# Kernel optimization log

Hardware: AMD Instinct MI355X
Metric: run time of the kernel (lower is better)

Reference implementation:

```python
import jax, jax.numpy as jnp
import numpy as np

F = 128          # feature_size
N = 512          # num_vertices (batch_size fixed to 1 by the original indexing)
C = 32 * 7 * 7 * 7   # 10976, f2 channel dim
G = 13           # f2 spatial grid (indices = (v+1)*6 in [0,12])
EPS = 1e-5


def _block(x, W1, b1, W2, b2, g, be, m, v):
    # Linear -> ELU -> Linear -> ELU -> Dropout(eval=id) -> BatchNorm1d(eval)
    h = jax.nn.elu(x @ W1 + b1)
    h = jax.nn.elu(h @ W2 + b2)
    return (h - m) * (g * jax.lax.rsqrt(v + EPS)) + be


def setup_inputs() -> dict:
    key = jax.random.key(0)
    ks = iter(jax.random.split(key, 80))

    def nrm(sh, s):
        return jax.random.normal(next(ks), sh, jnp.float32) * s

    def lin(i, o):
        return nrm((i, o), 1.0 / np.sqrt(i)), nrm((o,), 0.01)

    def bn():
        g = 1.0 + nrm((F,), 0.05)
        be = nrm((F,), 0.05)
        m = nrm((F,), 0.1)
        v = jax.random.uniform(next(ks), (F,), jnp.float32) + 0.5
        return g, be, m, v

    d = {}
    d['vertices'] = jax.random.uniform(next(ks), (1, N, 3), jnp.float32) * 2.0 - 1.0
    d['f2'] = nrm((1, G, G, G, C), 0.1)
    ii = jnp.arange(N, dtype=jnp.int32)
    d['v1s_idx'] = jnp.repeat(ii, N)   # edge k=(i,j): i = k//N
    d['v2s_idx'] = jnp.tile(ii, N)     #               j = k%N
    d['adj'] = (jax.random.uniform(next(ks), (N, N)) < 0.05).astype(jnp.float32)

    for p, (i, o) in [('mv', (3, F)), ('mf', (C, F)), ('s1', (2 * F, F)),
                      ('s2', (F, F)), ('s3', (2 * F, F))]:
        W1, b1 = lin(i, o)
        W2, b2 = lin(F, F)
        g, be, m, v = bn()
        d.update({p + '_W1': W1, p + '_b1': b1, p + '_W2': W2, p + '_b2': b2,
                  p + '_g': g, p + '_be': be, p + '_m': m, p + '_v': v})
    W3, b3 = lin(F, 2)
    d['s3_W3'], d['s3_b3'] = W3, b3
    return d


def _forward(vertices, f2, adj,
             mv_W1, mv_b1, mv_W2, mv_b2, mv_g, mv_be, mv_m, mv_v,
             mf_W1, mf_b1, mf_W2, mf_b2, mf_g, mf_be, mf_m, mf_v,
             s1_W1, s1_b1, s1_W2, s1_b2, s1_g, s1_be, s1_m, s1_v,
             s2_W1, s2_b1, s2_W2, s2_b2, s2_g, s2_be, s2_m, s2_v,
             s3_W1, s3_b1, s3_W2, s3_b2, s3_g, s3_be, s3_m, s3_v, s3_W3, s3_b3,
             v1s_idx, v2s_idx):
    b, n, _ = vertices.shape
    flat = vertices.reshape(-1, 3)                        # (B*N, 3)
    idx = ((flat + 1.0) * 6.0).astype(jnp.int32)          # grid indices in [0,12]
    f2e = f2[0, idx[:, 0], idx[:, 1], idx[:, 2], :]       # gather: (B*N, C)
    vf = _block(flat, mv_W1, mv_b1, mv_W2, mv_b2, mv_g, mv_be, mv_m, mv_v)
    ff = _block(f2e, mf_W1, mf_b1, mf_W2, mf_b2, mf_g, mf_be, mf_m, mf_v)
    vert = jnp.concatenate([vf, ff], -1).reshape(b, n, 2 * F)  # (B, N, 2F)

    # stage1: NodeToEdge (endpoint combine) -> MLP block over all N^2 edges
    e1 = vert[:, v1s_idx] + vert[:, v2s_idx]              # (B, N*N, 2F)
    s1 = _block(e1, s1_W1, s1_b1, s1_W2, s1_b2, s1_g, s1_be, s1_m, s1_v)  # (B, E, F)

    # stage2: EdgeToNode (adjacency-masked sum) -> MLP -> NodeToEdge
    nodes = jnp.einsum('bijf,ij->bif', s1.reshape(b, n, n, F), adj)  # (B, N, F)
    n2 = _block(nodes, s2_W1, s2_b1, s2_W2, s2_b2, s2_g, s2_be, s2_m, s2_v)
    s2 = n2[:, v1s_idx] + n2[:, v2s_idx]                  # (B, E, F)

    cat = jnp.concatenate([s1, s2], -1).reshape(b * n * n, 2 * F)
    h = _block(cat, s3_W1, s3_b1, s3_W2, s3_b2, s3_g, s3_be, s3_m, s3_v)
    return (h @ s3_W3 + s3_b3).reshape(b, n, n, 2)


def reference(vertices, f2, v1s_idx, v2s_idx, adj,
              mv_W1, mv_b1, mv_W2, mv_b2, mv_g, mv_be, mv_m, mv_v,
              mf_W1, mf_b1, mf_W2, mf_b2, mf_g, mf_be, mf_m, mf_v,
              s1_W1, s1_b1, s1_W2, s1_b2, s1_g, s1_be, s1_m, s1_v,
              s2_W1, s2_b1, s2_W2, s2_b2, s2_g, s2_be, s2_m, s2_v,
              s3_W1, s3_b1, s3_W2, s3_b2, s3_g, s3_be, s3_m, s3_v, s3_W3, s3_b3):
    return _forward(vertices, f2, adj,
                    mv_W1, mv_b1, mv_W2, mv_b2, mv_g, mv_be, mv_m, mv_v,
                    mf_W1, mf_b1, mf_W2, mf_b2, mf_g, mf_be, mf_m, mf_v,
                    s1_W1, s1_b1, s1_W2, s1_b2, s1_g, s1_be, s1_m, s1_v,
                    s2_W1, s2_b1, s2_W2, s2_b2, s2_g, s2_be, s2_m, s2_v,
                    s3_W1, s3_b1, s3_W2, s3_b2, s3_g, s3_be, s3_m, s3_v, s3_W3, s3_b3,
                    v1s_idx, v2s_idx)
```

## Files before the change

### kernel.cpp

```cpp
#include <hip/hip_runtime.h>
#include <hip/hip_bf16.h>


#define F    128
#define NV   512
#define CCC  10976
#define EPSV 1e-5f

typedef __attribute__((ext_vector_type(8)))  short        short8;
typedef __attribute__((ext_vector_type(4)))  float        f32x4;
typedef __attribute__((ext_vector_type(4)))  float        flt4;
typedef __attribute__((ext_vector_type(4)))  unsigned int u32x4;

union Frag { u32x4 q; short8 s; unsigned int d[4]; unsigned short u[8]; };

__device__ __forceinline__ unsigned short f2bf(float x){
  union { float f; unsigned int u; } c; c.f = x;
  unsigned int r = c.u + 0x7FFFu + ((c.u >> 16) & 1u);
  return (unsigned short)(r >> 16);
}
__device__ __forceinline__ unsigned int pkbf(float a, float b){
  union { __hip_bfloat162 h; unsigned int u; } cv;
  cv.h = __float22bfloat162_rn(make_float2(a, b));
  return cv.u;
}
__device__ __forceinline__ float eluf(float x){
  return x > 0.f ? x : (__expf(x) - 1.f);
}
__device__ __forceinline__ f32x4 mfma16(short8 a, short8 b, f32x4 c){
  return __builtin_amdgcn_mfma_f32_16x16x32_bf16(a, b, c, 0, 0, 0);
}

#define WS_U      0u
#define WS_FFPRE  262144u
#define WS_NODES  524288u
#define WS_WPERM  786432u
#define WS_ADJS   1048576u
#define WS_CNT    1050624u
#define WS_PJ     1052672u
#define WS_VEC    1183744u
#define WS_W2FS1  1188864u
#define WS_W1AFS3 1221632u
#define WS_W2FS3  1254400u
#define WS_W3F    1287168u
#define WS_MFW1F  1291264u
#define WS_END    4101120u
#define WS_PART   4101120u
#define WS_PART_END 15373312u


__global__ __launch_bounds__(256) void k_setup(
    const float* s1W2, const float* s3W1, const float* s3W2, const float* s3W3,
    const float* __restrict__ mfW1,
    const float* s1g, const float* s1be, const float* s1m, const float* s1v,
    const float* s3g, const float* s3be, const float* s3m, const float* s3v,
    const float* s1b2, const float* s3b2, const float* __restrict__ adj,
    unsigned short* w2fs1, unsigned short* w1afs3, unsigned short* w2fs3,
    unsigned short* w3f, unsigned short* __restrict__ mfw1f,
    float* vec, float* zeroreg,
    unsigned short* __restrict__ pj, int* __restrict__ cntI,
    float* __restrict__ cntF)
{
  __shared__ float sm[32 * 132];
  __shared__ unsigned long long msk[8];
  int bid = blockIdx.x, tid = threadIdx.x;

  if (bid < 460){
    int t = bid * 256 + tid;
    if (t < 49152){
      int T = t >> 14, tt = t & 16383;
      int e = tt & 7, lane = (tt >> 3) & 63, grp = tt >> 9;
      int slot = (grp >> 3) * 32 + ((lane >> 4) & 3) * 8 + e;
      int col  = (grp & 7) * 16 + (lane & 15);
      float val;
      unsigned short* dst;
      if (T == 0){ dst = w2fs1; val = s1W2[slot * F + col]; }
      else {
        int kf = (slot & 7) * 16 + (slot >> 3);
        if (T == 1){
          float sc1 = s1g[kf] * rsqrtf(s1v[kf] + EPSV);
          dst = w1afs3; val = sc1 * s3W1[kf * F + col];
        } else {
          dst = w2fs3; val = s3W2[kf * F + col];
        }
      }
      dst[tt] = f2bf(val);
      return;
    }
    t -= 49152;
    if (t < 2048){
      int e = t & 7, lane = (t >> 3) & 63, ks = t >> 9;
      int slot = ks * 32 + ((lane >> 4) & 3) * 8 + e;
      int kf = (slot & 7) * 16 + (slot >> 3);
      int n = lane & 15;
      float sc3 = s3g[kf] * rsqrtf(s3v[kf] + EPSV);
      w3f[t] = f2bf(n < 2 ? sc3 * s3W3[kf * 2 + n] : 0.f);
      return;
    }
    t -= 2048;
    if (t < 1024){
      int f = t & 127, which = t >> 7;
      int s = (f & 15) * 8 + (f >> 4);
      switch (which){
        case 0: vec[512 + s] = s1b2[f]; break;
        case 1: vec[640 + s] = s3b2[f]; break;
        case 2: vec[768 + f] = s1g[f] * rsqrtf(s1v[f] + EPSV); break;
        case 3: vec[896 + f] = s1be[f] - s1m[f] * (s1g[f] * rsqrtf(s1v[f] + EPSV)); break;
        case 4: {
          float a = 0.f;
          for (int k = 0; k < F; ++k){
            float sc = s1g[k] * rsqrtf(s1v[k] + EPSV);
            a = fmaf(s1be[k] - s1m[k] * sc, s3W1[k * F + f], a);
          }
          vec[1024 + f] = a;
        } break;
        case 5: if (f < 16){
          float a = 0.f;
          if (f < 2){
            for (int k = 0; k < F; ++k){
              float sc = s3g[k] * rsqrtf(s3v[k] + EPSV);
              a = fmaf(s3be[k] - s3m[k] * sc, s3W3[k * 2 + f], a);
            }
          }
          vec[1152 + f] = a;
        } break;
        default: break;
      }
      return;
    }
    t -= 1024;
    if (t < 65536) zeroreg[t] = 0.f;
    return;
  }

  if (bid < 803){
    int ksg = bid - 460;
    const float* src = mfW1 + ksg * 32 * F;
    #pragma unroll
    for (int p = 0; p < 4; ++p){
      int g4 = tid + p * 256;
      int row = g4 >> 5, col = (g4 & 31) * 4;
      flt4 v = *(const flt4*)(src + row * F + col);
      *(flt4*)(sm + row * 132 + col) = v;
    }
    __syncthreads();
    unsigned int* dst = (unsigned int*)mfw1f + ksg * 2048;
    #pragma unroll
    for (int q2 = 0; q2 < 8; ++q2){
      int o = (tid * 8 + q2) * 2;
      int nt = o >> 9, lane = (o >> 3) & 63, e = o & 7;
      int k = (lane >> 4) * 8 + e;
      int n = nt * 16 + (lane & 15);
      dst[tid * 8 + q2] = pkbf(sm[k * 132 + n], sm[(k + 1) * 132 + n]);
    }
    return;
  }

  {
    int i = bid - 803, wv = tid >> 6, ln = tid & 63;
    bool p0 = adj[i * NV + tid] != 0.f;
    bool p1 = adj[i * NV + 256 + tid] != 0.f;
    unsigned long long m0 = __ballot(p0);
    unsigned long long m1 = __ballot(p1);
    if (ln == 0){ msk[wv] = m0; msk[4 + wv] = m1; }
    __syncthreads();
    int base0 = 0, base1 = 0, tot = 0;
    #pragma unroll
    for (int g = 0; g < 8; ++g){
      int c = __popcll(msk[g]);
      if (g < wv) base0 += c;
      if (g < 4 + wv) base1 += c;
      tot += c;
    }
    unsigned long long below = (1ull << ln) - 1ull;
    if (p0){
      int r = base0 + __popcll(m0 & below);
      if (r < 128) pj[i * 128 + r] = (unsigned short)tid;
    }
    if (p1){
      int r = base1 + __popcll(m1 & below);
      if (r < 128) pj[i * 128 + r] = (unsigned short)(256 + tid);
    }
    if (tid == 0){ cntI[i] = tot > 128 ? 128 : tot; cntF[i] = (float)tot; }
  }
}

__global__ __launch_bounds__(256) void k_ff1(
    const float* __restrict__ verts, const float* __restrict__ f2,
    const unsigned short* __restrict__ mfw1f, float* __restrict__ ffpre,
    float* __restrict__ partials, int use_parts)
{
  int tid = threadIdx.x, w = tid >> 6, l = tid & 63, g = l >> 4, mm = l & 15;
  int mb = blockIdx.x & 7, kc = blockIdx.x >> 3;
  int v = mb * 64 + w * 16 + mm;
  float x0 = verts[v * 3 + 0], x1 = verts[v * 3 + 1], x2 = verts[v * 3 + 2];
  int i0 = (int)((x0 + 1.f) * 6.f), i1 = (int)((x1 + 1.f) * 6.f), i2 = (int)((x2 + 1.f) * 6.f);
  int base = ((i0 * 13 + i1) * 13 + i2) * CCC;

  f32x4 zero = {0.f, 0.f, 0.f, 0.f};
  f32x4 acc[8];
  #pragma unroll
  for (int nt = 0; nt < 8; ++nt) acc[nt] = zero;

  const u32x4* bt = (const u32x4*)mfw1f;
  #pragma unroll
  for (int kk = 0; kk < 8; ++kk){
    int ksg = kc * 8 + kk;
    if (ksg >= 343) break;
    const float* ap = f2 + base + ksg * 32 + g * 8;
    flt4 a0 = *(const flt4*)ap;
    flt4 a1 = *(const flt4*)(ap + 4);
    Frag a;
    a.d[0] = pkbf(a0.x, a0.y); a.d[1] = pkbf(a0.z, a0.w);
    a.d[2] = pkbf(a1.x, a1.y); a.d[3] = pkbf(a1.z, a1.w);
    #pragma unroll
    for (int nt = 0; nt < 8; ++nt){
      Frag b; b.q = bt[(ksg * 8 + nt) * 64 + l];
      acc[nt] = mfma16(a.s, b.s, acc[nt]);
    }
  }
  if (use_parts){
    #pragma unroll
    for (int nt = 0; nt < 8; ++nt){
      int n = nt * 16 + mm;
      #pragma unroll
      for (int r = 0; r < 4; ++r)
        partials[(kc * NV + mb * 64 + w * 16 + g * 4 + r) * F + n] = acc[nt][r];
    }
  } else {
    #pragma unroll
    for (int nt = 0; nt < 8; ++nt){
      int n = nt * 16 + mm;
      #pragma unroll
      for (int r = 0; r < 4; ++r)
        atomicAdd(&ffpre[(mb * 64 + w * 16 + g * 4 + r) * F + n], acc[nt][r]);
    }
  }
}

__global__ __launch_bounds__(128) void k_vert(
    const float* __restrict__ verts, const float* __restrict__ ffpre,
    const float* __restrict__ partials, int use_parts,
    const float* mvW1, const float* mvb1, const float* mvW2, const float* mvb2,
    const float* mvg, const float* mvbe, const float* mvm, const float* mvv,
    const float* mfb1, const float* mfW2, const float* mfb2,
    const float* mfg, const float* mfbe, const float* mfm, const float* mfv,
    const float* s1W1, const float* s1b1, float* __restrict__ uP)
{
  __shared__ float hv[F], hf[F], vf[F], ff[F];
  int f = threadIdx.x, v = blockIdx.x;
  float x0 = verts[v * 3], x1 = verts[v * 3 + 1], x2 = verts[v * 3 + 2];
  hv[f] = eluf(mvb1[f] + x0 * mvW1[f] + x1 * mvW1[F + f] + x2 * mvW1[2 * F + f]);
  float fp;
  if (use_parts){
    fp = 0.f;
    for (int kc = 0; kc < 43; ++kc) fp += partials[(kc * NV + v) * F + f];
  } else {
    fp = ffpre[v * F + f];
  }
  hf[f] = eluf(fp + mfb1[f]);
  __syncthreads();
  float sv = mvb2[f], sf = mfb2[f];
  for (int k = 0; k < F; ++k){
    sv = fmaf(hv[k], mvW2[k * F + f], sv);
    sf = fmaf(hf[k], mfW2[k * F + f], sf);
  }
  vf[f] = (eluf(sv) - mvm[f]) * (mvg[f] * rsqrtf(mvv[f] + EPSV)) + mvbe[f];
  ff[f] = (eluf(sf) - mfm[f]) * (mfg[f] * rsqrtf(mfv[f] + EPSV)) + mfbe[f];
  __syncthreads();
  float u = 0.5f * s1b1[f];
  for (int k = 0; k < F; ++k){
    u = fmaf(vf[k], s1W1[k * F + f], u);
    u = fmaf(ff[k], s1W1[(128 + k) * F + f], u);
  }
  uP[v * F + f] = u;
}

__global__ __launch_bounds__(256) void k_pass1s(
    const float* __restrict__ uP, const unsigned short* __restrict__ w2fs1,
    const float* __restrict__ vec, const unsigned short* __restrict__ pj,
    const int* __restrict__ cntA, float* __restrict__ nodes)
{
  __shared__ u32x4 Wb[2048];
  __shared__ float ci[F], nblk[F];
  int tid = threadIdx.x, i = blockIdx.x;
  int cnt = cntA[i];
  { const u32x4* ws_ = (const u32x4*)w2fs1;
    #pragma unroll
    for (int ii = 0; ii < 8; ++ii) Wb[tid + 256 * ii] = ws_[tid + 256 * ii]; }
  if (tid < F){ ci[tid] = uP[i * F + tid]; nblk[tid] = 0.f; }
  __syncthreads();

  int w = tid >> 6, l = tid & 63, g = l >> 4, mm = l & 15;
  float b2v[8];
  *(flt4*)&b2v[0] = *(const flt4*)(vec + 512 + mm * 8);
  *(flt4*)&b2v[4] = *(const flt4*)(vec + 516 + mm * 8);

  for (int t = 0; t * 64 < cnt; ++t){
    int row = t * 64 + w * 16 + mm;
    int j = (row < cnt) ? (int)pj[i * 128 + row] : 0;
    f32x4 acc[8];
    #pragma unroll
    for (int nt = 0; nt < 8; ++nt){ float b = b2v[nt]; acc[nt] = (f32x4){b, b, b, b}; }
    #pragma unroll
    for (int ks = 0; ks < 4; ++ks){
      int kb = ks * 32 + g * 8;
      flt4 ua = *(const flt4*)(uP + j * F + kb);
      flt4 ub = *(const flt4*)(uP + j * F + kb + 4);
      flt4 c0 = *(const flt4*)&ci[kb];
      flt4 c1 = *(const flt4*)&ci[kb + 4];
      Frag a;
      a.d[0] = pkbf(eluf(ua.x + c0.x), eluf(ua.y + c0.y));
      a.d[1] = pkbf(eluf(ua.z + c0.z), eluf(ua.w + c0.w));
      a.d[2] = pkbf(eluf(ub.x + c1.x), eluf(ub.y + c1.y));
      a.d[3] = pkbf(eluf(ub.z + c1.z), eluf(ub.w + c1.w));
      #pragma unroll
      for (int nt = 0; nt < 8; ++nt){
        Frag b; b.q = Wb[(ks * 8 + nt) * 64 + l];
        acc[nt] = mfma16(a.s, b.s, acc[nt]);
      }
    }
    int rbase = t * 64 + w * 16 + g * 4;
    float mk[4];
    #pragma unroll
    for (int r = 0; r < 4; ++r) mk[r] = (rbase + r < cnt) ? 1.f : 0.f;
    #pragma unroll
    for (int nt = 0; nt < 8; ++nt){
      float s = mk[0] * eluf(acc[nt][0]);
      s = fmaf(mk[1], eluf(acc[nt][1]), s);
      s = fmaf(mk[2], eluf(acc[nt][2]), s);
      s = fmaf(mk[3], eluf(acc[nt][3]), s);
      s += __shfl_xor(s, 16, 64);
      s += __shfl_xor(s, 32, 64);
      if (l < 16) atomicAdd(&nblk[nt * 16 + mm], s);
    }
  }
  __syncthreads();
  if (tid < F) nodes[i * F + tid] = nblk[tid];
}

__global__ __launch_bounds__(128) void k_mid(
    const float* __restrict__ nodes, const float* __restrict__ cntF,
    const float* __restrict__ vec,
    const float* s2W1, const float* s2b1, const float* s2W2, const float* s2b2,
    const float* s2g, const float* s2be, const float* s2m, const float* s2v,
    const float* s3W1, const float* s3b1, float* __restrict__ wPp)
{
  __shared__ float a[F], b[F];
  int f = threadIdx.x, r = blockIdx.x;
  a[f] = vec[768 + f] * nodes[r * F + f] + vec[896 + f] * cntF[r];
  __syncthreads();
  float s = s2b1[f];
  for (int k = 0; k < F; ++k) s = fmaf(a[k], s2W1[k * F + f], s);
  b[f] = eluf(s);
  __syncthreads();
  float s2 = s2b2[f];
  for (int k = 0; k < F; ++k) s2 = fmaf(b[k], s2W2[k * F + f], s2);
  float n2 = (eluf(s2) - s2m[f]) * (s2g[f] * rsqrtf(s2v[f] + EPSV)) + s2be[f];
  __syncthreads();
  a[f] = n2;
  __syncthreads();
  float wv = 0.5f * (s3b1[f] + vec[1024 + f]);
  for (int k = 0; k < F; ++k) wv = fmaf(a[k], s3W1[(128 + k) * F + f], wv);
  wPp[r * F + ((f & 15) * 8 + (f >> 4))] = wv;
}

__global__ __launch_bounds__(256, 2) void k_pass3(
    const float* __restrict__ uP, const float* __restrict__ wPp,
    const unsigned short* __restrict__ w2fs1, const unsigned short* __restrict__ w1afs3,
    const unsigned short* __restrict__ w2fs3, const unsigned short* __restrict__ w3f,
    const float* __restrict__ vec, const float* __restrict__ s3b3,
    float* __restrict__ out)
{
  __shared__ u32x4 Wb[2048];
  __shared__ __align__(16) char Hb[32768];
  __shared__ float ci[F];
  int tid = threadIdx.x, bid = blockIdx.x;
  int band, idx;
  if (bid < 512)      { band = 0; idx = bid; }
  else if (bid < 896) { band = 1; idx = bid - 512; }
  else if (bid < 1152){ band = 2; idx = bid - 896; }
  else                { band = 3; idx = bid - 1152; }
  int tpb = 4 - band;
  int i  = band * 128 + idx / tpb;
  int j0 = (band + idx % tpb) * 128;

  int w = tid >> 6, l = tid & 63, g = l >> 4, mm = l & 15;
  char* hb = Hb + w * 8192;
  int jbase = j0 + w * 32;
  int sx = (mm & 7) << 4;

  { const u32x4* ws_ = (const u32x4*)w2fs1;
    #pragma unroll
    for (int ii = 0; ii < 8; ++ii) Wb[tid + 256 * ii] = ws_[tid + 256 * ii]; }
  if (tid < F) ci[tid] = uP[i * F + tid];
  __syncthreads();

  f32x4 acc[2][8];
  {
    float b2v[8];
    *(flt4*)&b2v[0] = *(const flt4*)(vec + 512 + mm * 8);
    *(flt4*)&b2v[4] = *(const flt4*)(vec + 516 + mm * 8);
    #pragma unroll
    for (int m = 0; m < 2; ++m)
    #pragma unroll
    for (int nt = 0; nt < 8; ++nt){ float b = b2v[nt]; acc[m][nt] = (f32x4){b, b, b, b}; }
  }
  #pragma unroll
  for (int ks = 0; ks < 4; ++ks){
    int kb = ks * 32 + g * 8;
    flt4 c0 = *(const flt4*)&ci[kb];
    flt4 c1 = *(const flt4*)&ci[kb + 4];
    Frag a0, a1;
    {
      const float* p0 = uP + (jbase + mm) * F + kb;
      flt4 ua = *(const flt4*)p0;
      flt4 ub = *(const flt4*)(p0 + 4);
      a0.d[0] = pkbf(eluf(ua.x + c0.x), eluf(ua.y + c0.y));
      a0.d[1] = pkbf(eluf(ua.z + c0.z), eluf(ua.w + c0.w));
      a0.d[2] = pkbf(eluf(ub.x + c1.x), eluf(ub.y + c1.y));
      a0.d[3] = pkbf(eluf(ub.z + c1.z), eluf(ub.w + c1.w));
      const float* p1 = uP + (jbase + 16 + mm) * F + kb;
      flt4 va = *(const flt4*)p1;
      flt4 vb = *(const flt4*)(p1 + 4);
      a1.d[0] = pkbf(eluf(va.x + c0.x), eluf(va.y + c0.y));
      a1.d[1] = pkbf(eluf(va.z + c0.z), eluf(va.w + c0.w));
      a1.d[2] = pkbf(eluf(vb.x + c1.x), eluf(vb.y + c1.y));
      a1.d[3] = pkbf(eluf(vb.z + c1.z), eluf(vb.w + c1.w));
    }
    #pragma unroll
    for (int nt = 0; nt < 8; ++nt){
      Frag b; b.q = Wb[(ks * 8 + nt) * 64 + l];
      acc[0][nt] = mfma16(a0.s, b.s, acc[0][nt]);
      acc[1][nt] = mfma16(a1.s, b.s, acc[1][nt]);
    }
  }
  #pragma unroll
  for (int m = 0; m < 2; ++m)
  #pragma unroll
  for (int r = 0; r < 4; ++r){
    int row = m * 16 + g * 4 + r;
    u32x4 wd;
    #pragma unroll
    for (int q = 0; q < 4; ++q)
      wd[q] = pkbf(eluf(acc[m][2*q][r]), eluf(acc[m][2*q+1][r]));
    *(u32x4*)(hb + row * 256 + ((mm * 16) ^ ((row & 7) << 4))) = wd;
  }
  __syncthreads();
  { const u32x4* ws_ = (const u32x4*)w1afs3;
    #pragma unroll
    for (int ii = 0; ii < 8; ++ii) Wb[tid + 256 * ii] = ws_[tid + 256 * ii]; }
  __syncthreads();

  {
    float wiv[8];
    *(flt4*)&wiv[0] = *(const flt4*)(wPp + i * F + mm * 8);
    *(flt4*)&wiv[4] = *(const flt4*)(wPp + i * F + mm * 8 + 4);
    #pragma unroll
    for (int m = 0; m < 2; ++m)
    #pragma unroll
    for (int nt = 0; nt < 8; ++nt){ float b = wiv[nt]; acc[m][nt] = (f32x4){b, b, b, b}; }
  }
  #pragma unroll
  for (int ks = 0; ks < 4; ++ks){
    Frag a0; a0.q = *(const u32x4*)(hb + mm * 256 + ((ks * 64 + g * 16) ^ sx));
    Frag a1; a1.q = *(const u32x4*)(hb + (16 + mm) * 256 + ((ks * 64 + g * 16) ^ sx));
    #pragma unroll
    for (int nt = 0; nt < 8; ++nt){
      Frag b; b.q = Wb[(ks * 8 + nt) * 64 + l];
      acc[0][nt] = mfma16(a0.s, b.s, acc[0][nt]);
      acc[1][nt] = mfma16(a1.s, b.s, acc[1][nt]);
    }
  }
  #pragma unroll
  for (int m = 0; m < 2; ++m)
  #pragma unroll
  for (int r = 0; r < 4; ++r){
    int row = m * 16 + g * 4 + r;
    int jj = jbase + row;
    float wjv[8];
    *(flt4*)&wjv[0] = *(const flt4*)(wPp + jj * F + mm * 8);
    *(flt4*)&wjv[4] = *(const flt4*)(wPp + jj * F + mm * 8 + 4);
    u32x4 wd;
    #pragma unroll
    for (int q = 0; q < 4; ++q)
      wd[q] = pkbf(eluf(acc[m][2*q][r] + wjv[2*q]), eluf(acc[m][2*q+1][r] + wjv[2*q+1]));
    *(u32x4*)(hb + row * 256 + ((mm * 16) ^ ((row & 7) << 4))) = wd;
  }
  __syncthreads();
  { const u32x4* ws_ = (const u32x4*)w2fs3;
    #pragma unroll
    for (int ii = 0; ii < 8; ++ii) Wb[tid + 256 * ii] = ws_[tid + 256 * ii]; }
  __syncthreads();

  {
    float b2v[8];
    *(flt4*)&b2v[0] = *(const flt4*)(vec + 640 + mm * 8);
    *(flt4*)&b2v[4] = *(const flt4*)(vec + 644 + mm * 8);
    #pragma unroll
    for (int m = 0; m < 2; ++m)
    #pragma unroll
    for (int nt = 0; nt < 8; ++nt){ float b = b2v[nt]; acc[m][nt] = (f32x4){b, b, b, b}; }
  }
  #pragma unroll
  for (int ks = 0; ks < 4; ++ks){
    Frag a0; a0.q = *(const u32x4*)(hb + mm * 256 + ((ks * 64 + g * 16) ^ sx));
    Frag a1; a1.q = *(const u32x4*)(hb + (16 + mm) * 256 + ((ks * 64 + g * 16) ^ sx));
    #pragma unroll
    for (int nt = 0; nt < 8; ++nt){
      Frag b; b.q = Wb[(ks * 8 + nt) * 64 + l];
      acc[0][nt] = mfma16(a0.s, b.s, acc[0][nt]);
      acc[1][nt] = mfma16(a1.s, b.s, acc[1][nt]);
    }
  }
  #pragma unroll
  for (int m = 0; m < 2; ++m)
  #pragma unroll
  for (int r = 0; r < 4; ++r){
    int row = m * 16 + g * 4 + r;
    u32x4 wd;
    #pragma unroll
    for (int q = 0; q < 4; ++q)
      wd[q] = pkbf(eluf(acc[m][2*q][r]), eluf(acc[m][2*q+1][r]));
    *(u32x4*)(hb + row * 256 + ((mm * 16) ^ ((row & 7) << 4))) = wd;
  }

  float bb = (mm < 2) ? (s3b3[mm] + vec[1152 + mm]) : 0.f;
  f32x4 acc4[2] = {{bb, bb, bb, bb}, {bb, bb, bb, bb}};
  {
    const u32x4* w3q = (const u32x4*)w3f;
    #pragma unroll
    for (int ks = 0; ks < 4; ++ks){
      Frag a0; a0.q = *(const u32x4*)(hb + mm * 256 + ((ks * 64 + g * 16) ^ sx));
      Frag a1; a1.q = *(const u32x4*)(hb + (16 + mm) * 256 + ((ks * 64 + g * 16) ^ sx));
      Frag b; b.q = w3q[ks * 64 + l];
      acc4[0] = mfma16(a0.s, b.s, acc4[0]);
      acc4[1] = mfma16(a1.s, b.s, acc4[1]);
    }
  }
  if (mm < 2){
    #pragma unroll
    for (int m = 0; m < 2; ++m)
    #pragma unroll
    for (int r = 0; r < 4; ++r){
      int jr = jbase + m * 16 + g * 4 + r;
      if (jr >= i){
        float val = acc4[m][r];
        out[(i * NV + jr) * 2 + mm] = val;
        out[(jr * NV + i) * 2 + mm] = val;
      }
    }
  }
}

extern "C" void kernel_launch(void* const* d_in, const int* in_sizes, int n_in,
                              void* d_out, int out_size, void* d_ws, size_t ws_size,
                              hipStream_t stream)
{
  (void)in_sizes; (void)n_in; (void)out_size;
  const float* vertices = (const float*)d_in[0];
  const float* f2   = (const float*)d_in[1];
  const float* adj  = (const float*)d_in[4];
  const float* mvW1 = (const float*)d_in[5];
  const float* mvb1 = (const float*)d_in[6];
  const float* mvW2 = (const float*)d_in[7];
  const float* mvb2 = (const float*)d_in[8];
  const float* mvg  = (const float*)d_in[9];
  const float* mvbe = (const float*)d_in[10];
  const float* mvm  = (const float*)d_in[11];
  const float* mvv  = (const float*)d_in[12];
  const float* mfW1 = (const float*)d_in[13];
  const float* mfb1 = (const float*)d_in[14];
  const float* mfW2 = (const float*)d_in[15];
  const float* mfb2 = (const float*)d_in[16];
  const float* mfg  = (const float*)d_in[17];
  const float* mfbe = (const float*)d_in[18];
  const float* mfm  = (const float*)d_in[19];
  const float* mfv  = (const float*)d_in[20];
  const float* s1W1 = (const float*)d_in[21];
  const float* s1b1 = (const float*)d_in[22];
  const float* s1W2 = (const float*)d_in[23];
  const float* s1b2 = (const float*)d_in[24];
  const float* s1g  = (const float*)d_in[25];
  const float* s1be = (const float*)d_in[26];
  const float* s1m  = (const float*)d_in[27];
  const float* s1v  = (const float*)d_in[28];
  const float* s2W1 = (const float*)d_in[29];
  const float* s2b1 = (const float*)d_in[30];
  const float* s2W2 = (const float*)d_in[31];
  const float* s2b2 = (const float*)d_in[32];
  const float* s2g  = (const float*)d_in[33];
  const float* s2be = (const float*)d_in[34];
  const float* s2m  = (const float*)d_in[35];
  const float* s2v  = (const float*)d_in[36];
  const float* s3W1 = (const float*)d_in[37];
  const float* s3b1 = (const float*)d_in[38];
  const float* s3W2 = (const float*)d_in[39];
  const float* s3b2 = (const float*)d_in[40];
  const float* s3g  = (const float*)d_in[41];
  const float* s3be = (const float*)d_in[42];
  const float* s3m  = (const float*)d_in[43];
  const float* s3v  = (const float*)d_in[44];
  const float* s3W3 = (const float*)d_in[45];
  const float* s3b3 = (const float*)d_in[46];

  char* ws = (char*)d_ws;
  float* uP    = (float*)(ws + WS_U);
  float* ffpre = (float*)(ws + WS_FFPRE);
  float* nodes = (float*)(ws + WS_NODES);
  float* wPp   = (float*)(ws + WS_WPERM);
  float* cntF  = (float*)(ws + WS_ADJS);
  int*   cntI  = (int*)(ws + WS_CNT);
  unsigned short* pj = (unsigned short*)(ws + WS_PJ);
  float* vec   = (float*)(ws + WS_VEC);
  unsigned short* w2fs1  = (unsigned short*)(ws + WS_W2FS1);
  unsigned short* w1afs3 = (unsigned short*)(ws + WS_W1AFS3);
  unsigned short* w2fs3  = (unsigned short*)(ws + WS_W2FS3);
  unsigned short* w3f    = (unsigned short*)(ws + WS_W3F);
  unsigned short* mfw1f  = (unsigned short*)(ws + WS_MFW1F);
  float* parts = (float*)(ws + WS_PART);
  int use_parts = (ws_size >= (size_t)WS_PART_END) ? 1 : 0;

  k_setup<<<1315, 256, 0, stream>>>(s1W2, s3W1, s3W2, s3W3, mfW1,
      s1g, s1be, s1m, s1v, s3g, s3be, s3m, s3v, s1b2, s3b2, adj,
      w2fs1, w1afs3, w2fs3, w3f, mfw1f, vec, ffpre, pj, cntI, cntF);
  k_ff1<<<344, 256, 0, stream>>>(vertices, f2, mfw1f, ffpre, parts, use_parts);
  k_vert<<<512, 128, 0, stream>>>(vertices, ffpre, parts, use_parts,
      mvW1, mvb1, mvW2, mvb2, mvg, mvbe, mvm, mvv,
      mfb1, mfW2, mfb2, mfg, mfbe, mfm, mfv,
      s1W1, s1b1, uP);
  k_pass1s<<<512, 256, 0, stream>>>(uP, w2fs1, vec, pj, cntI, nodes);
  k_mid<<<512, 128, 0, stream>>>(nodes, cntF, vec,
      s2W1, s2b1, s2W2, s2b2, s2g, s2be, s2m, s2v, s3W1, s3b1, wPp);
  k_pass3<<<1280, 256, 0, stream>>>(uP, wPp, w2fs1, w1afs3, w2fs3, w3f, vec,
      s3b3, (float*)d_out);
}
```

Baseline: 109.6 us.

## Make pass3 persistent with all three weight matrices resident in LDS

k_pass3 now launches 256 blocks of 512 threads that stay resident. Each block loads the three 128x128 bf16 weight matrices into shared memory once, and each wave then loops over 32-row work units. Work units lying entirely below the diagonal are skipped, and the per-stage __syncthreads between weight reloads are removed. The intent is to cut repeated weight traffic and barrier stalls, at the cost of much larger LDS use per block (96KB weights plus 64KB H buffer), which limits occupancy and may not allow two blocks per CU.

```diff
diff --git a/kernel.cpp b/kernel.cpp
--- a/kernel.cpp
+++ b/kernel.cpp
@@ -365,189 +365,189 @@
   wPp[r * F + ((f & 15) * 8 + (f >> 4))] = wv;
 }
 
-__global__ __launch_bounds__(256, 2) void k_pass3(
+__global__ __launch_bounds__(512, 2) void k_pass3(
     const float* __restrict__ uP, const float* __restrict__ wPp,
     const unsigned short* __restrict__ w2fs1, const unsigned short* __restrict__ w1afs3,
     const unsigned short* __restrict__ w2fs3, const unsigned short* __restrict__ w3f,
     const float* __restrict__ vec, const float* __restrict__ s3b3,
     float* __restrict__ out)
 {
-  __shared__ u32x4 Wb[2048];
-  __shared__ __align__(16) char Hb[32768];
-  __shared__ float ci[F];
-  int tid = threadIdx.x, bid = blockIdx.x;
-  int band, idx;
-  if (bid < 512)      { band = 0; idx = bid; }
-  else if (bid < 896) { band = 1; idx = bid - 512; }
-  else if (bid < 1152){ band = 2; idx = bid - 896; }
-  else                { band = 3; idx = bid - 1152; }
-  int tpb = 4 - band;
-  int i  = band * 128 + idx / tpb;
-  int j0 = (band + idx % tpb) * 128;
+  __shared__ u32x4 Wall[6144];
+  __shared__ __align__(16) char Hb[65536];
+  int tid = threadIdx.x;
+  {
+    const u32x4* p0 = (const u32x4*)w2fs1;
+    const u32x4* p1 = (const u32x4*)w1afs3;
+    const u32x4* p2 = (const u32x4*)w2fs3;
+    #pragma unroll
+    for (int ii = 0; ii < 4; ++ii){
+      Wall[       tid + 512 * ii] = p0[tid + 512 * ii];
+      Wall[2048 + tid + 512 * ii] = p1[tid + 512 * ii];
+      Wall[4096 + tid + 512 * ii] = p2[tid + 512 * ii];
+    }
+  }
+  __syncthreads();
 
   int w = tid >> 6, l = tid & 63, g = l >> 4, mm = l & 15;
   char* hb = Hb + w * 8192;
-  int jbase = j0 + w * 32;
   int sx = (mm & 7) << 4;
 
-  { const u32x4* ws_ = (const u32x4*)w2fs1;
-    #pragma unroll
-    for (int ii = 0; ii < 8; ++ii) Wb[tid + 256 * ii] = ws_[tid + 256 * ii]; }
-  if (tid < F) ci[tid] = uP[i * F + tid];
-  __syncthreads();
-
-  f32x4 acc[2][8];
-  {
-    float b2v[8];
-    *(flt4*)&b2v[0] = *(const flt4*)(vec + 512 + mm * 8);
-    *(flt4*)&b2v[4] = *(const flt4*)(vec + 516 + mm * 8);
+  float b2v1[8], b2v3[8];
+  *(flt4*)&b2v1[0] = *(const flt4*)(vec + 512 + mm * 8);
+  *(flt4*)&b2v1[4] = *(const flt4*)(vec + 516 + mm * 8);
+  *(flt4*)&b2v3[0] = *(const flt4*)(vec + 640 + mm * 8);
+  *(flt4*)&b2v3[4] = *(const flt4*)(vec + 644 + mm * 8);
+  float bb = (mm < 2) ? (s3b3[mm] + vec[1152 + mm]) : 0.f;
+
+  for (int jb = blockIdx.x * 8 + w; jb < 5120; jb += 2048){
+    int tile = jb >> 2, sub = jb & 3;
+    int band, idx;
+    if (tile < 512)      { band = 0; idx = tile; }
+    else if (tile < 896) { band = 1; idx = tile - 512; }
+    else if (tile < 1152){ band = 2; idx = tile - 896; }
+    else                 { band = 3; idx = tile - 1152; }
+    int tpb = 4 - band;
+    int i  = band * 128 + idx / tpb;
+    int jbase = (band + idx % tpb) * 128 + sub * 32;
+    if (jbase + 32 <= i) continue;
+
+    flt4 c0[4], c1[4];
+    #pragma unroll
+    for (int ks = 0; ks < 4; ++ks){
+      c0[ks] = *(const flt4*)(uP + i * F + ks * 32 + g * 8);
+      c1[ks] = *(const flt4*)(uP + i * F + ks * 32 + g * 8 + 4);
+    }
+
+    f32x4 acc[2][8];
     #pragma unroll
     for (int m = 0; m < 2; ++m)
     #pragma unroll
-    for (int nt = 0; nt < 8; ++nt){ float b = b2v[nt]; acc[m][nt] = (f32x4){b, b, b, b}; }
-  }
-  #pragma unroll
-  for (int ks = 0; ks < 4; ++ks){
-    int kb = ks * 32 + g * 8;
-    flt4 c0 = *(const flt4*)&ci[kb];
-    flt4 c1 = *(const flt4*)&ci[kb + 4];
-    Frag a0, a1;
+    for (int nt = 0; nt < 8; ++nt){ float b = b2v1[nt]; acc[m][nt] = (f32x4){b, b, b, b}; }
+    #pragma unroll
+    for (int ks = 0; ks < 4; ++ks){
+      int kb = ks * 32 + g * 8;
+      Frag a0, a1;
+      {
+        const float* p0 = uP + (jbase + mm) * F + kb;
+        flt4 ua = *(const flt4*)p0;
+        flt4 ub = *(const flt4*)(p0 + 4);
+        a0.d[0] = pkbf(eluf(ua.x + c0[ks].x), eluf(ua.y + c0[ks].y));
+        a0.d[1] = pkbf(eluf(ua.z + c0[ks].z), eluf(ua.w + c0[ks].w));
+        a0.d[2] = pkbf(eluf(ub.x + c1[ks].x), eluf(ub.y + c1[ks].y));
+        a0.d[3] = pkbf(eluf(ub.z + c1[ks].z), eluf(ub.w + c1[ks].w));
+        const float* p1 = uP + (jbase + 16 + mm) * F + kb;
+        flt4 va = *(const flt4*)p1;
+        flt4 vb = *(const flt4*)(p1 + 4);
+        a1.d[0] = pkbf(eluf(va.x + c0[ks].x), eluf(va.y + c0[ks].y));
+        a1.d[1] = pkbf(eluf(va.z + c0[ks].z), eluf(va.w + c0[ks].w));
+        a1.d[2] = pkbf(eluf(vb.x + c1[ks].x), eluf(vb.y + c1[ks].y));
+        a1.d[3] = pkbf(eluf(vb.z + c1[ks].z), eluf(vb.w + c1[ks].w));
+      }
+      #pragma unroll
+      for (int nt = 0; nt < 8; ++nt){
+        Frag b; b.q = Wall[(ks * 8 + nt) * 64 + l];
+        acc[0][nt] = mfma16(a0.s, b.s, acc[0][nt]);
+        acc[1][nt] = mfma16(a1.s, b.s, acc[1][nt]);
+      }
+    }
+    #pragma unroll
+    for (int m = 0; m < 2; ++m)
+    #pragma unroll
+    for (int r = 0; r < 4; ++r){
+      int row = m * 16 + g * 4 + r;
+      u32x4 wd;
+      #pragma unroll
+      for (int q = 0; q < 4; ++q)
+        wd[q] = pkbf(eluf(acc[m][2*q][r]), eluf(acc[m][2*q+1][r]));
+      *(u32x4*)(hb + row * 256 + ((mm * 16) ^ ((row & 7) << 4))) = wd;
+    }
+
     {
-      const float* p0 = uP + (jbase + mm) * F + kb;
-      flt4 ua = *(const flt4*)p0;
-      flt4 ub = *(const flt4*)(p0 + 4);
-      a0.d[0] = pkbf(eluf(ua.x + c0.x), eluf(ua.y + c0.y));
-      a0.d[1] = pkbf(eluf(ua.z + c0.z), eluf(ua.w + c0.w));
-      a0.d[2] = pkbf(eluf(ub.x + c1.x), eluf(ub.y + c1.y));
-      a0.d[3] = pkbf(eluf(ub.z + c1.z), eluf(ub.w + c1.w));
-      const float* p1 = uP + (jbase + 16 + mm) * F + kb;
-      flt4 va = *(const flt4*)p1;
-      flt4 vb = *(const flt4*)(p1 + 4);
-      a1.d[0] = pkbf(eluf(va.x + c0.x), eluf(va.y + c0.y));
-      a1.d[1] = pkbf(eluf(va.z + c0.z), eluf(va.w + c0.w));
-      a1.d[2] = pkbf(eluf(vb.x + c1.x), eluf(vb.y + c1.y));
-      a1.d[3] = pkbf(eluf(vb.z + c1.z), eluf(vb.w + c1.w));
-    }
-    #pragma unroll
-    for (int nt = 0; nt < 8; ++nt){
-      Frag b; b.q = Wb[(ks * 8 + nt) * 64 + l];
-      acc[0][nt] = mfma16(a0.s, b.s, acc[0][nt]);
-      acc[1][nt] = mfma16(a1.s, b.s, acc[1][nt]);
-    }
-  }
-  #pragma unroll
-  for (int m = 0; m < 2; ++m)
-  #pragma unroll
-  for (int r = 0; r < 4; ++r){
-    int row = m * 16 + g * 4 + r;
-    u32x4 wd;
-    #pragma unroll
-    for (int q = 0; q < 4; ++q)
-      wd[q] = pkbf(eluf(acc[m][2*q][r]), eluf(acc[m][2*q+1][r]));
-    *(u32x4*)(hb + row * 256 + ((mm * 16) ^ ((row & 7) << 4))) = wd;
-  }
-  __syncthreads();
-  { const u32x4* ws_ = (const u32x4*)w1afs3;
-    #pragma unroll
-    for (int ii = 0; ii < 8; ++ii) Wb[tid + 256 * ii] = ws_[tid + 256 * ii]; }
-  __syncthreads();
-
-  {
-    float wiv[8];
-    *(flt4*)&wiv[0] = *(const flt4*)(wPp + i * F + mm * 8);
-    *(flt4*)&wiv[4] = *(const flt4*)(wPp + i * F + mm * 8 + 4);
-    #pragma unroll
-    for (int m = 0; m < 2; ++m)
-    #pragma unroll
-    for (int nt = 0; nt < 8; ++nt){ float b = wiv[nt]; acc[m][nt] = (f32x4){b, b, b, b}; }
-  }
-  #pragma unroll
-  for (int ks = 0; ks < 4; ++ks){
-    Frag a0; a0.q = *(const u32x4*)(hb + mm * 256 + ((ks * 64 + g * 16) ^ sx));
-    Frag a1; a1.q = *(const u32x4*)(hb + (16 + mm) * 256 + ((ks * 64 + g * 16) ^ sx));
-    #pragma unroll
-    for (int nt = 0; nt < 8; ++nt){
-      Frag b; b.q = Wb[(ks * 8 + nt) * 64 + l];
-      acc[0][nt] = mfma16(a0.s, b.s, acc[0][nt]);
-      acc[1][nt] = mfma16(a1.s, b.s, acc[1][nt]);
-    }
-  }
-  #pragma unroll
-  for (int m = 0; m < 2; ++m)
-  #pragma unroll
-  for (int r = 0; r < 4; ++r){
-    int row = m * 16 + g * 4 + r;
-    int jj = jbase + row;
-    float wjv[8];
-    *(flt4*)&wjv[0] = *(const flt4*)(wPp + jj * F + mm * 8);
-    *(flt4*)&wjv[4] = *(const flt4*)(wPp + jj * F + mm * 8 + 4);
-    u32x4 wd;
-    #pragma unroll
-    for (int q = 0; q < 4; ++q)
-      wd[q] = pkbf(eluf(acc[m][2*q][r] + wjv[2*q]), eluf(acc[m][2*q+1][r] + wjv[2*q+1]));
-    *(u32x4*)(hb + row * 256 + ((mm * 16) ^ ((row & 7) << 4))) = wd;
-  }
-  __syncthreads();
-  { const u32x4* ws_ = (const u32x4*)w2fs3;
-    #pragma unroll
-    for (int ii = 0; ii < 8; ++ii) Wb[tid + 256 * ii] = ws_[tid + 256 * ii]; }
-  __syncthreads();
-
-  {
-    float b2v[8];
-    *(flt4*)&b2v[0] = *(const flt4*)(vec + 640 + mm * 8);
-    *(flt4*)&b2v[4] = *(const flt4*)(vec + 644 + mm * 8);
-    #pragma unroll
-    for (int m = 0; m < 2; ++m)
-    #pragma unroll
-    for (int nt = 0; nt < 8; ++nt){ float b = b2v[nt]; acc[m][nt] = (f32x4){b, b, b, b}; }
-  }
-  #pragma unroll
-  for (int ks = 0; ks < 4; ++ks){
-    Frag a0; a0.q = *(const u32x4*)(hb + mm * 256 + ((ks * 64 + g * 16) ^ sx));
-    Frag a1; a1.q = *(const u32x4*)(hb + (16 + mm) * 256 + ((ks * 64 + g * 16) ^ sx));
-    #pragma unroll
-    for (int nt = 0; nt < 8; ++nt){
-      Frag b; b.q = Wb[(ks * 8 + nt) * 64 + l];
-      acc[0][nt] = mfma16(a0.s, b.s, acc[0][nt]);
-      acc[1][nt] = mfma16(a1.s, b.s, acc[1][nt]);
-    }
-  }
-  #pragma unroll
-  for (int m = 0; m < 2; ++m)
-  #pragma unroll
-  for (int r = 0; r < 4; ++r){
-    int row = m * 16 + g * 4 + r;
-    u32x4 wd;
-    #pragma unroll
-    for (int q = 0; q < 4; ++q)
-      wd[q] = pkbf(eluf(acc[m][2*q][r]), eluf(acc[m][2*q+1][r]));
-    *(u32x4*)(hb + row * 256 + ((mm * 16) ^ ((row & 7) << 4))) = wd;
-  }
-
-  float bb = (mm < 2) ? (s3b3[mm] + vec[1152 + mm]) : 0.f;
-  f32x4 acc4[2] = {{bb, bb, bb, bb}, {bb, bb, bb, bb}};
-  {
-    const u32x4* w3q = (const u32x4*)w3f;
+      float wiv[8];
+      *(flt4*)&wiv[0] = *(const flt4*)(wPp + i * F + mm * 8);
+      *(flt4*)&wiv[4] = *(const flt4*)(wPp + i * F + mm * 8 + 4);
+      #pragma unroll
+      for (int m = 0; m < 2; ++m)
+      #pragma unroll
+      for (int nt = 0; nt < 8; ++nt){ float b = wiv[nt]; acc[m][nt] = (f32x4){b, b, b, b}; }
+    }
     #pragma unroll
     for (int ks = 0; ks < 4; ++ks){
       Frag a0; a0.q = *(const u32x4*)(hb + mm * 256 + ((ks * 64 + g * 16) ^ sx));
       Frag a1; a1.q = *(const u32x4*)(hb + (16 + mm) * 256 + ((ks * 64 + g * 16) ^ sx));
-      Frag b; b.q = w3q[ks * 64 + l];
-      acc4[0] = mfma16(a0.s, b.s, acc4[0]);
-      acc4[1] = mfma16(a1.s, b.s, acc4[1]);
-    }
-  }
-  if (mm < 2){
+      #pragma unroll
+      for (int nt = 0; nt < 8; ++nt){
+        Frag b; b.q = Wall[2048 + (ks * 8 + nt) * 64 + l];
+        acc[0][nt] = mfma16(a0.s, b.s, acc[0][nt]);
+        acc[1][nt] = mfma16(a1.s, b.s, acc[1][nt]);
+      }
+    }
     #pragma unroll
     for (int m = 0; m < 2; ++m)
     #pragma unroll
     for (int r = 0; r < 4; ++r){
-      int jr = jbase + m * 16 + g * 4 + r;
-      if (jr >= i){
-        float val = acc4[m][r];
-        out[(i * NV + jr) * 2 + mm] = val;
-        out[(jr * NV + i) * 2 + mm] = val;
+      int row = m * 16 + g * 4 + r;
+      int jj = jbase + row;
+      float wjv[8];
+      *(flt4*)&wjv[0] = *(const flt4*)(wPp + jj * F + mm * 8);
+      *(flt4*)&wjv[4] = *(const flt4*)(wPp + jj * F + mm * 8 + 4);
+      u32x4 wd;
+      #pragma unroll
+      for (int q = 0; q < 4; ++q)
+        wd[q] = pkbf(eluf(acc[m][2*q][r] + wjv[2*q]), eluf(acc[m][2*q+1][r] + wjv[2*q+1]));
+      *(u32x4*)(hb + row * 256 + ((mm * 16) ^ ((row & 7) << 4))) = wd;
+    }
+
+    #pragma unroll
+    for (int m = 0; m < 2; ++m)
+    #pragma unroll
+    for (int nt = 0; nt < 8; ++nt){ float b = b2v3[nt]; acc[m][nt] = (f32x4){b, b, b, b}; }
+    #pragma unroll
+    for (int ks = 0; ks < 4; ++ks){
+      Frag a0; a0.q = *(const u32x4*)(hb + mm * 256 + ((ks * 64 + g * 16) ^ sx));
+      Frag a1; a1.q = *(const u32x4*)(hb + (16 + mm) * 256 + ((ks * 64 + g * 16) ^ sx));
+      #pragma unroll
+      for (int nt = 0; nt < 8; ++nt){
+        Frag b; b.q = Wall[4096 + (ks * 8 + nt) * 64 + l];
+        acc[0][nt] = mfma16(a0.s, b.s, acc[0][nt]);
+        acc[1][nt] = mfma16(a1.s, b.s, acc[1][nt]);
+      }
+    }
+    #pragma unroll
+    for (int m = 0; m < 2; ++m)
+    #pragma unroll
+    for (int r = 0; r < 4; ++r){
+      int row = m * 16 + g * 4 + r;
+      u32x4 wd;
+      #pragma unroll
+      for (int q = 0; q < 4; ++q)
+        wd[q] = pkbf(eluf(acc[m][2*q][r]), eluf(acc[m][2*q+1][r]));
+      *(u32x4*)(hb + row * 256 + ((mm * 16) ^ ((row & 7) << 4))) = wd;
+    }
+
+    f32x4 acc4[2] = {{bb, bb, bb, bb}, {bb, bb, bb, bb}};
+    {
+      const u32x4* w3q = (const u32x4*)w3f;
+      #pragma unroll
+      for (int ks = 0; ks < 4; ++ks){
+        Frag a0; a0.q = *(const u32x4*)(hb + mm * 256 + ((ks * 64 + g * 16) ^ sx));
+        Frag a1; a1.q = *(const u32x4*)(hb + (16 + mm) * 256 + ((ks * 64 + g * 16) ^ sx));
+        Frag b; b.q = w3q[ks * 64 + l];
+        acc4[0] = mfma16(a0.s, b.s, acc4[0]);
+        acc4[1] = mfma16(a1.s, b.s, acc4[1]);
+      }
+    }
+    if (mm < 2){
+      #pragma unroll
+      for (int m = 0; m < 2; ++m)
+      #pragma unroll
+      for (int r = 0; r < 4; ++r){
+        int jr = jbase + m * 16 + g * 4 + r;
+        if (jr >= i){
+          float val = acc4[m][r];
+          out[(i * NV + jr) * 2 + mm] = val;
+          out[(jr * NV + i) * 2 + mm] = val;
+        }
       }
     }
   }
@@ -632,6 +632,6 @@
   k_pass1s<<<512, 256, 0, stream>>>(uP, w2fs1, vec, pj, cntI, nodes);
   k_mid<<<512, 128, 0, stream>>>(nodes, cntF, vec,
       s2W1, s2b1, s2W2, s2b2, s2g, s2be, s2m, s2v, s3W1, s3b1, wPp);
-  k_pass3<<<1280, 256, 0, stream>>>(uP, wPp, w2fs1, w1afs3, w2fs3, w3f, vec,
+  k_pass3<<<256, 512, 0, stream>>>(uP, wPp, w2fs1, w1afs3, w2fs3, w3f, vec,
       s3b3, (float*)d_out);
 }
```

Result: no change. 111.2 us (+1.5%).
